# Kernel tuning notes

Measured on AMD Instinct MI355X. Metric: run time of the kernel, lower is better.

Reference implementation:

```python
import jax, jax.numpy as jnp
import numpy as np

B, C, H, W = 2, 256, 64, 64
D = 4  # max dilation ring


def _offsets():
    offs = [(0, 0)]
    for s in range(1, D + 1):
        for a in (-s, 0, s):
            for b in (-s, 0, s):
                if a != 0 or b != 0:
                    offs.append((a, b))
    return np.array(offs, dtype=np.int32)  # (33, 2)


def setup_inputs() -> dict:
    key = jax.random.key(0)
    k1, k2, k3, k4 = jax.random.split(key, 4)
    scale = 1.0 / np.sqrt(C)
    return {
        "Ft": jax.random.normal(k1, (B, C, H, W), dtype=jnp.float32),
        "Ft_epsilon": jax.random.normal(k2, (B, C, H, W), dtype=jnp.float32),
        "Wf": jax.random.normal(k3, (256, C), dtype=jnp.float32) * scale,
        "bf": jnp.zeros((256,), dtype=jnp.float32),
        "Wg": jax.random.normal(k4, (256, C), dtype=jnp.float32) * scale,
        "bg": jnp.zeros((256,), dtype=jnp.float32),
    }


def reference(Ft, Ft_epsilon, Wf, bf, Wg, bg):
    # 1x1 conv embeddings
    Ef = jnp.einsum("bchw,oc->bohw", Ft, Wf) + bf[None, :, None, None]          # f(Ft)
    Eg = jnp.einsum("bchw,oc->bohw", Ft_epsilon, Wg) + bg[None, :, None, None]  # g(Ft_eps)

    offs = _offsets()                                  # (K,2), K=33
    dx = jnp.asarray(offs[:, 0])[:, None, None]        # (K,1,1)
    dy = jnp.asarray(offs[:, 1])[:, None, None]
    xs = jnp.arange(H)[None, :, None] + dx             # (K,H,1)
    ys = jnp.arange(W)[None, None, :] + dy             # (K,1,W)
    valid = ((xs >= 0) & (xs < H)) & ((ys >= 0) & (ys < W))  # (K,H,W)
    xc = jnp.clip(xs, 0, H - 1)
    yc = jnp.clip(ys, 0, W - 1)

    # gather neighbor embeddings and features: (B,C,K,H,W)
    Ef_n = Ef[:, :, xc, yc]
    Ft_n = Ft[:, :, xc, yc]

    # affinity of center embedding with each neighbor embedding
    aff = jnp.einsum("bchw,bckhw->bkhw", Eg, Ef_n)     # (B,K,H,W)
    aff = jnp.where(valid[None], aff, -jnp.inf)        # clip out-of-bounds neighbors
    w = jax.nn.softmax(aff, axis=1)                    # (B,K,H,W); center always valid

    out = jnp.einsum("bkhw,bckhw->bchw", w, Ft_n)      # (B,C,H,W)
    return out
```

## Files before the change

kernel.cpp:

```cpp
#include <hip/hip_runtime.h>
#include <math.h>

typedef __attribute__((ext_vector_type(4))) float f4;

__device__ __forceinline__ int iclamp(int x, int lo, int hi) { return min(max(x, lo), hi); }

__device__ constexpr int DXC[33] = {0, -1,-1,-1,0,0,1,1,1, -2,-2,-2,0,0,2,2,2, -3,-3,-3,0,0,3,3,3, -4,-4,-4,0,0,4,4,4};
__device__ constexpr int DYC[33] = {0, -1,0,1,-1,1,-1,0,1, -2,0,2,-2,2,-2,0,2, -3,0,3,-3,3,-3,0,3, -4,0,4,-4,4,-4,0,4};

__global__ __launch_bounds__(256, 2) void gemm_f32(
    const float* __restrict__ Wf, const float* __restrict__ bf,
    const float* __restrict__ Wg, const float* __restrict__ bg,
    const float* __restrict__ Ft, const float* __restrict__ FtE,
    float* __restrict__ Ef, float* __restrict__ Eg)
{
    __shared__ float As[2][32][132];
    __shared__ float Bs[2][32][64];

    const int bn = blockIdx.x, bm = blockIdx.y, gb = blockIdx.z;
    const int g = gb >> 1, b = gb & 1;
    const float* Wmat = g ? Wg : Wf;
    const float* bias = g ? bg : bf;
    const float* X = (g ? FtE : Ft) + (size_t)b * 256 * 4096;
    float* E = (g ? Eg : Ef) + (size_t)b * 256 * 4096;

    const int tid = threadIdx.x;
    const int tn = tid & 15, tm = tid >> 4;
    const int m0 = bm * 128, n0 = bn * 64;

    float acc[8][4] = {};
    f4 areg[4], breg[2];

    auto loadA = [&](int kk) {
        #pragma unroll
        for (int i = 0; i < 4; ++i) {
            int f = i * 256 + tid, m = f >> 3, cq = f & 7;
            areg[i] = *(const f4*)&Wmat[(m0 + m) * 256 + kk + cq * 4];
        }
    };
    auto loadB = [&](int kk) {
        #pragma unroll
        for (int i = 0; i < 2; ++i) {
            int f = i * 256 + tid, c = f >> 4, n4 = f & 15;
            breg[i] = *(const f4*)&X[(size_t)(kk + c) * 4096 + n0 + n4 * 4];
        }
    };
    auto storeLDS = [&](int buf) {
        #pragma unroll
        for (int i = 0; i < 4; ++i) {
            int f = i * 256 + tid, m = f >> 3, cq = f & 7;
            As[buf][cq * 4 + 0][m] = areg[i].x;
            As[buf][cq * 4 + 1][m] = areg[i].y;
            As[buf][cq * 4 + 2][m] = areg[i].z;
            As[buf][cq * 4 + 3][m] = areg[i].w;
        }
        #pragma unroll
        for (int i = 0; i < 2; ++i) {
            int f = i * 256 + tid, c = f >> 4, n4 = f & 15;
            *(f4*)&Bs[buf][c][n4 * 4] = breg[i];
        }
    };

    loadA(0); loadB(0); storeLDS(0);
    __syncthreads();

    for (int ch = 0; ch < 8; ++ch) {
        const int buf = ch & 1;
        if (ch < 7) { loadA((ch + 1) * 32); loadB((ch + 1) * 32); }
        #pragma unroll 4
        for (int k = 0; k < 32; ++k) {
            f4 a0 = *(const f4*)&As[buf][k][tm * 8];
            f4 a1 = *(const f4*)&As[buf][k][tm * 8 + 4];
            f4 bb = *(const f4*)&Bs[buf][k][tn * 4];
            #pragma unroll
            for (int ii = 0; ii < 4; ++ii)
                #pragma unroll
                for (int jj = 0; jj < 4; ++jj) {
                    acc[ii][jj]     += a0[ii] * bb[jj];
                    acc[4 + ii][jj] += a1[ii] * bb[jj];
                }
        }
        if (ch < 7) storeLDS(buf ^ 1);
        __syncthreads();
    }

    #pragma unroll
    for (int r = 0; r < 8; ++r) {
        int o = m0 + tm * 8 + r;
        float bvs = bias[o];
        f4 v = { acc[r][0] + bvs, acc[r][1] + bvs, acc[r][2] + bvs, acc[r][3] + bvs };
        *(f4*)&E[(size_t)o * 4096 + n0 + tn * 4] = v;
    }
}

template<int K0, int NK>
__device__ __forceinline__ void aff_accum(const float* __restrict__ base, float* __restrict__ aff)
{
    #pragma unroll
    for (int ch = 0; ch < 8; ++ch) {
        float eg = base[(72 + ch) * 72];
        #pragma unroll
        for (int j = 0; j < NK; ++j) {
            constexpr int kk0 = K0;
            int k = kk0 + j;
            aff[j] += eg * base[((DXC[k] + 4) * 8 + ch) * 72 + DYC[k]];
        }
    }
}

__global__ __launch_bounds__(256, 2) void aff_part(
    const float* __restrict__ Ef, const float* __restrict__ Eg,
    float* __restrict__ part)
{
    __shared__ float L[2][10 * 8 * 72];

    const int h = blockIdx.x, b = blockIdx.y, cseg = blockIdx.z;
    const int tid = threadIdx.x;
    const int w = tid & 63, kg = tid >> 6;
    const size_t plane = (size_t)b * 256 * 4096;
    const float* EfB = Ef + plane;
    const float* EgB = Eg + plane;
    const int cbase = cseg * 64;

    int hr[10];
    #pragma unroll
    for (int d = 0; d < 10; ++d) hr[d] = (d < 9) ? iclamp(h + d - 4, 0, 63) : h;

    f4 vreg[5]; float sreg[3];

    auto load_rnd = [&](int r) {
        const int c0 = cbase + r * 8;
        #pragma unroll
        for (int i = 0; i < 5; ++i) {
            int f = i * 256 + tid, d = f >> 7, rem = f & 127, ch = rem >> 4, c4 = rem & 15;
            const float* src = (d < 9) ? EfB : EgB;
            vreg[i] = *(const f4*)&src[(size_t)(c0 + ch) * 4096 + hr[d] * 64 + c4 * 4];
        }
        #pragma unroll
        for (int i = 0; i < 3; ++i) {
            int e = i * 256 + tid;
            if (e < 640) {
                int row = e >> 3, sc = e & 7, d = row >> 3, ch = row & 7;
                int wsrc = (sc < 4) ? 0 : 63;
                const float* src = (d < 9) ? EfB : EgB;
                sreg[i] = src[(size_t)(c0 + ch) * 4096 + hr[d] * 64 + wsrc];
            }
        }
    };
    auto store_rnd = [&](int buf) {
        float* Lb = L[buf];
        #pragma unroll
        for (int i = 0; i < 5; ++i) {
            int f = i * 256 + tid, d = f >> 7, rem = f & 127, ch = rem >> 4, c4 = rem & 15;
            *(f4*)&Lb[(d * 8 + ch) * 72 + 4 + c4 * 4] = vreg[i];
        }
        #pragma unroll
        for (int i = 0; i < 3; ++i) {
            int e = i * 256 + tid;
            if (e < 640) {
                int row = e >> 3, sc = e & 7, d = row >> 3, ch = row & 7;
                int col = (sc < 4) ? sc : (64 + sc);
                Lb[(d * 8 + ch) * 72 + col] = sreg[i];
            }
        }
    };

    float aff[9] = {0.f,0.f,0.f,0.f,0.f,0.f,0.f,0.f,0.f};

    load_rnd(0); store_rnd(0);
    for (int r = 0; r < 8; ++r) {
        if (r < 7) load_rnd(r + 1);
        __syncthreads();
        const float* base = &L[r & 1][4 + w];
        switch (kg) {
            case 0: aff_accum<0, 9>(base, aff); break;
            case 1: aff_accum<9, 8>(base, aff); break;
            case 2: aff_accum<17, 8>(base, aff); break;
            default: aff_accum<25, 8>(base, aff); break;
        }
        if (r < 7) store_rnd((r + 1) & 1);
    }

    const int k0 = (kg == 0) ? 0 : (kg == 1) ? 9 : (kg == 2) ? 17 : 25;
    const int nk = (kg == 0) ? 9 : 8;
    float* pB = part + (((size_t)cseg * 2 + b) * 33) * 4096 + h * 64 + w;
    for (int j = 0; j < nk; ++j) pB[(size_t)(k0 + j) * 4096] = aff[j];
}

__global__ __launch_bounds__(256, 2) void softmax_k(
    const float* __restrict__ part, float* __restrict__ wgt)
{
    const int id = blockIdx.x * 256 + threadIdx.x;
    const int b = id >> 12, p = id & 4095;
    const int h = p >> 6, w = p & 63;

    float a[33];
    float m = -INFINITY;
    #pragma unroll
    for (int k = 0; k < 33; ++k) {
        float s = part[(((size_t)0 * 2 + b) * 33 + k) * 4096 + p]
                + part[(((size_t)1 * 2 + b) * 33 + k) * 4096 + p]
                + part[(((size_t)2 * 2 + b) * 33 + k) * 4096 + p]
                + part[(((size_t)3 * 2 + b) * 33 + k) * 4096 + p];
        bool valid = ((unsigned)(h + DXC[k]) < 64u) && ((unsigned)(w + DYC[k]) < 64u);
        a[k] = valid ? s : -INFINITY;
        m = fmaxf(m, a[k]);
    }
    float ssum = 0.f;
    #pragma unroll
    for (int k = 0; k < 33; ++k) { float e = __expf(a[k] - m); a[k] = e; ssum += e; }
    float inv = 1.0f / ssum;
    float* wgtB = wgt + (size_t)b * 33 * 4096 + p;
    #pragma unroll
    for (int k = 0; k < 33; ++k) wgtB[(size_t)k * 4096] = a[k] * inv;
}

__global__ __launch_bounds__(256, 2) void out_kernel(
    const float* __restrict__ wgt, const float* __restrict__ Ft,
    float* __restrict__ out)
{
    __shared__ float L[2][9 * 8 * 72];

    const int h = blockIdx.x, b = blockIdx.y, cseg = blockIdx.z;
    const int tid = threadIdx.x;
    const int w = tid & 63, cg = tid >> 6;
    const size_t plane = (size_t)b * 256 * 4096;
    const float* FtB = Ft + plane;
    float* outB = out + plane;
    const int cbase = cseg * 64;
    const int p = h * 64 + w;

    const float* wgtB = wgt + (size_t)b * 33 * 4096 + p;
    float wv[33];
    #pragma unroll
    for (int k = 0; k < 33; ++k) wv[k] = wgtB[(size_t)k * 4096];

    int hr[9];
    #pragma unroll
    for (int d = 0; d < 9; ++d) hr[d] = iclamp(h + d - 4, 0, 63);

    f4 vreg[5]; float sreg[3];

    auto load_rnd = [&](int r) {
        const int c0 = cbase + r * 8;
        #pragma unroll
        for (int i = 0; i < 5; ++i) {
            int f = i * 256 + tid;
            if (f < 1152) {
                int d = f >> 7, rem = f & 127, ch = rem >> 4, c4 = rem & 15;
                vreg[i] = *(const f4*)&FtB[(size_t)(c0 + ch) * 4096 + hr[d] * 64 + c4 * 4];
            }
        }
        #pragma unroll
        for (int i = 0; i < 3; ++i) {
            int e = i * 256 + tid;
            if (e < 576) {
                int row = e >> 3, sc = e & 7, d = row >> 3, ch = row & 7;
                int wsrc = (sc < 4) ? 0 : 63;
                sreg[i] = FtB[(size_t)(c0 + ch) * 4096 + hr[d] * 64 + wsrc];
            }
        }
    };
    auto store_rnd = [&](int buf) {
        float* Lb = L[buf];
        #pragma unroll
        for (int i = 0; i < 5; ++i) {
            int f = i * 256 + tid;
            if (f < 1152) {
                int d = f >> 7, rem = f & 127, ch = rem >> 4, c4 = rem & 15;
                *(f4*)&Lb[(d * 8 + ch) * 72 + 4 + c4 * 4] = vreg[i];
            }
        }
        #pragma unroll
        for (int i = 0; i < 3; ++i) {
            int e = i * 256 + tid;
            if (e < 576) {
                int row = e >> 3, sc = e & 7, d = row >> 3, ch = row & 7;
                int col = (sc < 4) ? sc : (64 + sc);
                Lb[(d * 8 + ch) * 72 + col] = sreg[i];
            }
        }
    };

    load_rnd(0); store_rnd(0);
    for (int r = 0; r < 8; ++r) {
        if (r < 7) load_rnd(r + 1);
        __syncthreads();
        const float* base = &L[r & 1][4 + w];
        #pragma unroll
        for (int u = 0; u < 2; ++u) {
            const float* b2 = base + (cg * 2 + u) * 72;
            float o = 0.f;
            #pragma unroll
            for (int k = 0; k < 33; ++k)
                o += wv[k] * b2[(DXC[k] + 4) * 576 + DYC[k]];
            int c = cbase + r * 8 + cg * 2 + u;
            outB[(size_t)c * 4096 + p] = o;
        }
        if (r < 7) store_rnd((r + 1) & 1);
    }
}

extern "C" void kernel_launch(void* const* d_in, const int* in_sizes, int n_in,
                              void* d_out, int out_size, void* d_ws, size_t ws_size,
                              hipStream_t stream) {
    const float* Ft  = (const float*)d_in[0];
    const float* FtE = (const float*)d_in[1];
    const float* Wf  = (const float*)d_in[2];
    const float* bf  = (const float*)d_in[3];
    const float* Wg  = (const float*)d_in[4];
    const float* bg  = (const float*)d_in[5];
    float* out = (float*)d_out;

    float* Ef  = (float*)d_ws;
    float* Eg  = Ef + (size_t)2 * 256 * 4096;
    float* part = Eg + (size_t)2 * 256 * 4096;
    float* wgt = part + (size_t)4 * 2 * 33 * 4096;

    hipLaunchKernelGGL(gemm_f32, dim3(64, 2, 4), dim3(256), 0, stream,
                       Wf, bf, Wg, bg, Ft, FtE, Ef, Eg);
    hipLaunchKernelGGL(aff_part, dim3(64, 2, 4), dim3(256), 0, stream,
                       Ef, Eg, part);
    hipLaunchKernelGGL(softmax_k, dim3(32), dim3(256), 0, stream,
                       part, wgt);
    hipLaunchKernelGGL(out_kernel, dim3(64, 2, 4), dim3(256), 0, stream,
                       wgt, Ft, out);
}
```

Before: 140.7 us.

## Fold the two embedding projections into one precomputed matrix and fuse the softmax

The two 1x1-conv embeddings are reassociated: a new small kernel computes M = Wf^T·Wg and r = Wf^T·bg, and a single GEMM then produces G = M·Ft_eps + r. The affinity is taken directly between neighbor Ft values and G. The bf term is constant across neighbors, so it cancels in the softmax and is dropped. This halves the large projection GEMM work and avoids writing Ef. Separately, the standalone softmax kernel is removed and its work is folded into out_kernel, overlapped with the first tile load; this costs an extra launch for mat_M and slightly different float rounding.

```diff
diff --git a/kernel.cpp b/kernel.cpp
--- a/kernel.cpp
+++ b/kernel.cpp
@@ -8,21 +8,67 @@
 __device__ constexpr int DXC[33] = {0, -1,-1,-1,0,0,1,1,1, -2,-2,-2,0,0,2,2,2, -3,-3,-3,0,0,3,3,3, -4,-4,-4,0,0,4,4,4};
 __device__ constexpr int DYC[33] = {0, -1,0,1,-1,1,-1,0,1, -2,0,2,-2,2,-2,0,2, -3,0,3,-3,3,-3,0,3, -4,0,4,-4,4,-4,0,4};
 
-__global__ __launch_bounds__(256, 2) void gemm_f32(
-    const float* __restrict__ Wf, const float* __restrict__ bf,
-    const float* __restrict__ Wg, const float* __restrict__ bg,
-    const float* __restrict__ Ft, const float* __restrict__ FtE,
-    float* __restrict__ Ef, float* __restrict__ Eg)
+__global__ __launch_bounds__(256) void mat_M(
+    const float* __restrict__ Wf, const float* __restrict__ Wg,
+    const float* __restrict__ bg, float* __restrict__ M, float* __restrict__ r)
+{
+    __shared__ float Sf[32][33], Sg[32][33];
+    __shared__ float Rs[32][9];
+    const int c1b = blockIdx.x * 32, c2b = blockIdx.y * 32;
+    const int tid = threadIdx.x;
+    const int tx = tid & 15, ty = tid >> 4;
+    float acc[2][2] = {};
+    for (int ko = 0; ko < 256; ko += 32) {
+        #pragma unroll
+        for (int i = 0; i < 4; ++i) {
+            int f = i * 256 + tid;
+            int o = f >> 5, c = f & 31;
+            Sf[o][c] = Wf[(ko + o) * 256 + c1b + c];
+            Sg[o][c] = Wg[(ko + o) * 256 + c2b + c];
+        }
+        __syncthreads();
+        #pragma unroll
+        for (int o = 0; o < 32; ++o) {
+            float f0 = Sf[o][ty * 2], f1 = Sf[o][ty * 2 + 1];
+            float g0 = Sg[o][tx * 2], g1 = Sg[o][tx * 2 + 1];
+            acc[0][0] += f0 * g0; acc[0][1] += f0 * g1;
+            acc[1][0] += f1 * g0; acc[1][1] += f1 * g1;
+        }
+        __syncthreads();
+    }
+    #pragma unroll
+    for (int i = 0; i < 2; ++i)
+        #pragma unroll
+        for (int j = 0; j < 2; ++j)
+            M[(size_t)(c1b + ty * 2 + i) * 256 + c2b + tx * 2 + j] = acc[i][j];
+
+    if (blockIdx.y == 0) {
+        const int c1l = tid & 31, og = tid >> 5;
+        float s = 0.f;
+        #pragma unroll 8
+        for (int o = og * 32; o < og * 32 + 32; ++o)
+            s += Wf[o * 256 + c1b + c1l] * bg[o];
+        Rs[c1l][og] = s;
+        __syncthreads();
+        if (tid < 32) {
+            float t = 0.f;
+            #pragma unroll
+            for (int j = 0; j < 8; ++j) t += Rs[tid][j];
+            r[c1b + tid] = t;
+        }
+    }
+}
+
+__global__ __launch_bounds__(256, 2) void gemm_G(
+    const float* __restrict__ M, const float* __restrict__ r,
+    const float* __restrict__ X0, float* __restrict__ G)
 {
     __shared__ float As[2][32][132];
     __shared__ float Bs[2][32][64];
 
-    const int bn = blockIdx.x, bm = blockIdx.y, gb = blockIdx.z;
-    const int g = gb >> 1, b = gb & 1;
-    const float* Wmat = g ? Wg : Wf;
-    const float* bias = g ? bg : bf;
-    const float* X = (g ? FtE : Ft) + (size_t)b * 256 * 4096;
-    float* E = (g ? Eg : Ef) + (size_t)b * 256 * 4096;
+    const int bn = blockIdx.x, bm = blockIdx.y, b = blockIdx.z;
+    const float* X = X0 + (size_t)b * 256 * 4096;
+    float* E = G + (size_t)b * 256 * 4096;
 
     const int tid = threadIdx.x;
     const int tn = tid & 15, tm = tid >> 4;
@@ -35,7 +81,7 @@
         #pragma unroll
         for (int i = 0; i < 4; ++i) {
             int f = i * 256 + tid, m = f >> 3, cq = f & 7;
-            areg[i] = *(const f4*)&Wmat[(m0 + m) * 256 + kk + cq * 4];
+            areg[i] = *(const f4*)&M[(m0 + m) * 256 + kk + cq * 4];
         }
     };
     auto loadB = [&](int kk) {
@@ -85,10 +131,10 @@
     }
 
     #pragma unroll
-    for (int r = 0; r < 8; ++r) {
-        int o = m0 + tm * 8 + r;
-        float bvs = bias[o];
-        f4 v = { acc[r][0] + bvs, acc[r][1] + bvs, acc[r][2] + bvs, acc[r][3] + bvs };
+    for (int rr = 0; rr < 8; ++rr) {
+        int o = m0 + tm * 8 + rr;
+        float bvs = r[o];
+        f4 v = { acc[rr][0] + bvs, acc[rr][1] + bvs, acc[rr][2] + bvs, acc[rr][3] + bvs };
         *(f4*)&E[(size_t)o * 4096 + n0 + tn * 4] = v;
     }
 }
@@ -109,7 +155,7 @@
 }
 
 __global__ __launch_bounds__(256, 2) void aff_part(
-    const float* __restrict__ Ef, const float* __restrict__ Eg,
+    const float* __restrict__ Ftg, const float* __restrict__ Gc,
     float* __restrict__ part)
 {
     __shared__ float L[2][10 * 8 * 72];
@@ -118,8 +164,8 @@
     const int tid = threadIdx.x;
     const int w = tid & 63, kg = tid >> 6;
     const size_t plane = (size_t)b * 256 * 4096;
-    const float* EfB = Ef + plane;
-    const float* EgB = Eg + plane;
+    const float* FtB = Ftg + plane;
+    const float* GB  = Gc + plane;
     const int cbase = cseg * 64;
 
     int hr[10];
@@ -128,12 +174,12 @@
 
     f4 vreg[5]; float sreg[3];
 
-    auto load_rnd = [&](int r) {
-        const int c0 = cbase + r * 8;
+    auto load_rnd = [&](int rr) {
+        const int c0 = cbase + rr * 8;
         #pragma unroll
         for (int i = 0; i < 5; ++i) {
             int f = i * 256 + tid, d = f >> 7, rem = f & 127, ch = rem >> 4, c4 = rem & 15;
-            const float* src = (d < 9) ? EfB : EgB;
+            const float* src = (d < 9) ? FtB : GB;
             vreg[i] = *(const f4*)&src[(size_t)(c0 + ch) * 4096 + hr[d] * 64 + c4 * 4];
         }
         #pragma unroll
@@ -142,7 +188,7 @@
             if (e < 640) {
                 int row = e >> 3, sc = e & 7, d = row >> 3, ch = row & 7;
                 int wsrc = (sc < 4) ? 0 : 63;
-                const float* src = (d < 9) ? EfB : EgB;
+                const float* src = (d < 9) ? FtB : GB;
                 sreg[i] = src[(size_t)(c0 + ch) * 4096 + hr[d] * 64 + wsrc];
             }
         }
@@ -168,17 +214,17 @@
     float aff[9] = {0.f,0.f,0.f,0.f,0.f,0.f,0.f,0.f,0.f};
 
     load_rnd(0); store_rnd(0);
-    for (int r = 0; r < 8; ++r) {
-        if (r < 7) load_rnd(r + 1);
-        __syncthreads();
-        const float* base = &L[r & 1][4 + w];
+    for (int rr = 0; rr < 8; ++rr) {
+        if (rr < 7) load_rnd(rr + 1);
+        __syncthreads();
+        const float* base = &L[rr & 1][4 + w];
         switch (kg) {
             case 0: aff_accum<0, 9>(base, aff); break;
             case 1: aff_accum<9, 8>(base, aff); break;
             case 2: aff_accum<17, 8>(base, aff); break;
             default: aff_accum<25, 8>(base, aff); break;
         }
-        if (r < 7) store_rnd((r + 1) & 1);
+        if (rr < 7) store_rnd((rr + 1) & 1);
     }
 
     const int k0 = (kg == 0) ? 0 : (kg == 1) ? 9 : (kg == 2) ? 17 : 25;
@@ -187,36 +233,8 @@
     for (int j = 0; j < nk; ++j) pB[(size_t)(k0 + j) * 4096] = aff[j];
 }
 
-__global__ __launch_bounds__(256, 2) void softmax_k(
-    const float* __restrict__ part, float* __restrict__ wgt)
-{
-    const int id = blockIdx.x * 256 + threadIdx.x;
-    const int b = id >> 12, p = id & 4095;
-    const int h = p >> 6, w = p & 63;
-
-    float a[33];
-    float m = -INFINITY;
-    #pragma unroll
-    for (int k = 0; k < 33; ++k) {
-        float s = part[(((size_t)0 * 2 + b) * 33 + k) * 4096 + p]
-                + part[(((size_t)1 * 2 + b) * 33 + k) * 4096 + p]
-                + part[(((size_t)2 * 2 + b) * 33 + k) * 4096 + p]
-                + part[(((size_t)3 * 2 + b) * 33 + k) * 4096 + p];
-        bool valid = ((unsigned)(h + DXC[k]) < 64u) && ((unsigned)(w + DYC[k]) < 64u);
-        a[k] = valid ? s : -INFINITY;
-        m = fmaxf(m, a[k]);
-    }
-    float ssum = 0.f;
-    #pragma unroll
-    for (int k = 0; k < 33; ++k) { float e = __expf(a[k] - m); a[k] = e; ssum += e; }
-    float inv = 1.0f / ssum;
-    float* wgtB = wgt + (size_t)b * 33 * 4096 + p;
-    #pragma unroll
-    for (int k = 0; k < 33; ++k) wgtB[(size_t)k * 4096] = a[k] * inv;
-}
-
 __global__ __launch_bounds__(256, 2) void out_kernel(
-    const float* __restrict__ wgt, const float* __restrict__ Ft,
+    const float* __restrict__ part, const float* __restrict__ Ft,
     float* __restrict__ out)
 {
     __shared__ float L[2][9 * 8 * 72];
@@ -230,19 +248,14 @@
     const int cbase = cseg * 64;
     const int p = h * 64 + w;
 
-    const float* wgtB = wgt + (size_t)b * 33 * 4096 + p;
-    float wv[33];
-    #pragma unroll
-    for (int k = 0; k < 33; ++k) wv[k] = wgtB[(size_t)k * 4096];
-
     int hr[9];
     #pragma unroll
     for (int d = 0; d < 9; ++d) hr[d] = iclamp(h + d - 4, 0, 63);
 
     f4 vreg[5]; float sreg[3];
 
-    auto load_rnd = [&](int r) {
-        const int c0 = cbase + r * 8;
+    auto load_rnd = [&](int rr) {
+        const int c0 = cbase + rr * 8;
         #pragma unroll
         for (int i = 0; i < 5; ++i) {
             int f = i * 256 + tid;
@@ -282,11 +295,34 @@
         }
     };
 
-    load_rnd(0); store_rnd(0);
-    for (int r = 0; r < 8; ++r) {
-        if (r < 7) load_rnd(r + 1);
-        __syncthreads();
-        const float* base = &L[r & 1][4 + w];
+    load_rnd(0);
+
+    float wv[33];
+    {
+        constexpr size_t CS = (size_t)2 * 33 * 4096;
+        const float* pB = part + ((size_t)b * 33) * 4096 + p;
+        float mx = -INFINITY;
+        #pragma unroll
+        for (int k = 0; k < 33; ++k) {
+            size_t off = (size_t)k * 4096;
+            float s = pB[off] + pB[CS + off] + pB[2 * CS + off] + pB[3 * CS + off];
+            bool valid = ((unsigned)(h + DXC[k]) < 64u) && ((unsigned)(w + DYC[k]) < 64u);
+            wv[k] = valid ? s : -INFINITY;
+            mx = fmaxf(mx, wv[k]);
+        }
+        float ssum = 0.f;
+        #pragma unroll
+        for (int k = 0; k < 33; ++k) { float e = __expf(wv[k] - mx); wv[k] = e; ssum += e; }
+        float inv = 1.0f / ssum;
+        #pragma unroll
+        for (int k = 0; k < 33; ++k) wv[k] *= inv;
+    }
+
+    store_rnd(0);
+    for (int rr = 0; rr < 8; ++rr) {
+        if (rr < 7) load_rnd(rr + 1);
+        __syncthreads();
+        const float* base = &L[rr & 1][4 + w];
         #pragma unroll
         for (int u = 0; u < 2; ++u) {
             const float* b2 = base + (cg * 2 + u) * 72;
@@ -294,10 +330,10 @@
             #pragma unroll
             for (int k = 0; k < 33; ++k)
                 o += wv[k] * b2[(DXC[k] + 4) * 576 + DYC[k]];
-            int c = cbase + r * 8 + cg * 2 + u;
+            int c = cbase + rr * 8 + cg * 2 + u;
             outB[(size_t)c * 4096 + p] = o;
         }
-        if (r < 7) store_rnd((r + 1) & 1);
+        if (rr < 7) store_rnd((rr + 1) & 1);
     }
 }
 
@@ -311,18 +347,19 @@
     const float* Wg  = (const float*)d_in[4];
     const float* bg  = (const float*)d_in[5];
     float* out = (float*)d_out;
-
-    float* Ef  = (float*)d_ws;
-    float* Eg  = Ef + (size_t)2 * 256 * 4096;
-    float* part = Eg + (size_t)2 * 256 * 4096;
-    float* wgt = part + (size_t)4 * 2 * 33 * 4096;
-
-    hipLaunchKernelGGL(gemm_f32, dim3(64, 2, 4), dim3(256), 0, stream,
-                       Wf, bf, Wg, bg, Ft, FtE, Ef, Eg);
+    (void)bf;
+
+    float* G    = (float*)d_ws;
+    float* part = G + (size_t)2 * 256 * 4096;
+    float* Mw   = part + (size_t)4 * 2 * 33 * 4096;
+    float* rw   = Mw + 256 * 256;
+
+    hipLaunchKernelGGL(mat_M, dim3(8, 8), dim3(256), 0, stream,
+                       Wf, Wg, bg, Mw, rw);
+    hipLaunchKernelGGL(gemm_G, dim3(64, 2, 2), dim3(256), 0, stream,
+                       Mw, rw, FtE, G);
     hipLaunchKernelGGL(aff_part, dim3(64, 2, 4), dim3(256), 0, stream,
-                       Ef, Eg, part);
-    hipLaunchKernelGGL(softmax_k, dim3(32), dim3(256), 0, stream,
-                       part, wgt);
+                       Ft, G, part);
     hipLaunchKernelGGL(out_kernel, dim3(64, 2, 4), dim3(256), 0, stream,
-                       wgt, Ft, out);
-}
+                       part, Ft, out);
+}
```

Result: slower. 143.7 us (+2.1%).
